# Optimization experiments

Measured on AMD Instinct MI355X. Metric: run time of the kernel, lower is better.

Reference implementation:

```python
import jax, jax.numpy as jnp
import numpy as np

B, T, D1, D2, DM, V, K = 2, 512, 256, 128, 1024, 32000, 4
SCALE = 0.05  # keep tanh/sigmoid out of full saturation with randn params


def setup_inputs() -> dict:
    key = jax.random.key(0)
    ks = jax.random.split(key, 7)
    s = lambda k, shape: SCALE * jax.random.normal(k, shape, dtype=jnp.float32)
    return {
        "gc": jax.random.normal(ks[0], (B, T, D1), dtype=jnp.float32),
        "H": s(ks[1], (K, DM, D1)),
        "U": s(ks[2], (K, D2, D1)),
        "v": s(ks[3], (V, D2)),
        "u": s(ks[4], (K, D1)),
        "b": s(ks[5], (V, K)),
        "emb": s(ks[6], (V, DM)),
    }


def reference(gc, H, U, v, u, b, emb):
    # gc: (B,T,D1)
    hc = jnp.tanh(jnp.einsum('kdi,bti->btkd', H, gc))        # (B,T,K,DM)
    tU = jnp.tanh(jnp.einsum('kji,bti->btkj', U, gc))        # (B,T,K,D2)
    # token- and context-dependent gate logits: (B,T,V,K)
    lc = (jnp.einsum('vj,btkj->btvk', v, tU)
          + jnp.einsum('ki,bti->btk', u, gc)[:, :, None, :]
          + b[None, None])
    gamma = jax.nn.sigmoid(lc[..., :K - 1])                  # (B,T,V,3)
    g0, g1, g2 = gamma[..., 0], gamma[..., 1], gamma[..., 2]
    # sigmoid-tree mixture priors: (B,T,V,K)
    pi = jnp.stack([g0 * g1, g0 * (1.0 - g1),
                    (1.0 - g0) * g2, (1.0 - g0) * (1.0 - g2)], axis=-1)
    # contract hc with embeddings per gate FIRST (avoids btikj blow-up),
    # then weight by pi -- same math as the original pi (x) emb outer product.
    dots = jnp.einsum('btkd,vd->btvk', hc, emb)              # (B,T,V,K)
    logits = jnp.sum(pi * dots, axis=-1)                     # (B,T,V)
    return jax.nn.softmax(logits, axis=-1)
```

## Files before the change

### kernel.cpp

```cpp
#include <hip/hip_runtime.h>
#include <math.h>

namespace {

typedef _Float16 f16;
typedef _Float16 f16x8 __attribute__((ext_vector_type(8)));
typedef float    f32x4 __attribute__((ext_vector_type(4)));

constexpr int kBT = 1024, kD1 = 256, kD2 = 128, kDM = 1024, kV = 32000, kK = 4;
constexpr int AR = kBT * kK;
constexpr int ROWS_H = kK * kDM;
constexpr int ROWS_U = kK * kD2;
constexpr int ROWS_ALL = ROWS_H + ROWS_U + kK;
constexpr int HALF_ROWS = ROWS_ALL / 2;

__global__ __launch_bounds__(256) void prep_gemm(
    const float* __restrict__ gc, const float* __restrict__ Hm,
    const float* __restrict__ Um, const float* __restrict__ um,
    f16* __restrict__ hc, f16* __restrict__ tu, float* __restrict__ ug)
{
    __shared__ float sgc[8][kD1];
    const int btBase = blockIdx.x * 8;
    for (int idx = threadIdx.x; idx < 8 * kD1; idx += 256)
        sgc[idx / kD1][idx % kD1] = gc[(size_t)btBase * kD1 + idx];
    __syncthreads();

    const int rStart = blockIdx.y * HALF_ROWS;
    const int rEnd   = rStart + HALF_ROWS;
    for (int r = rStart + (int)threadIdx.x; r < rEnd; r += 256) {
        const float* wrow;
        if (r < ROWS_H)               wrow = Hm + (size_t)r * kD1;
        else if (r < ROWS_H + ROWS_U) wrow = Um + (size_t)(r - ROWS_H) * kD1;
        else                          wrow = um + (size_t)(r - ROWS_H - ROWS_U) * kD1;

        float acc[8] = {0.f,0.f,0.f,0.f,0.f,0.f,0.f,0.f};
        for (int i = 0; i < kD1; i += 4) {
            const float4 w = *reinterpret_cast<const float4*>(wrow + i);
            #pragma unroll
            for (int b = 0; b < 8; ++b) {
                const float4 g = *reinterpret_cast<const float4*>(&sgc[b][i]);
                acc[b] = fmaf(w.x, g.x, acc[b]);
                acc[b] = fmaf(w.y, g.y, acc[b]);
                acc[b] = fmaf(w.z, g.z, acc[b]);
                acc[b] = fmaf(w.w, g.w, acc[b]);
            }
        }
        #pragma unroll
        for (int b = 0; b < 8; ++b) {
            const int bt = btBase + b;
            if (r < ROWS_H) {
                const int k = r >> 10, d = r & 1023;
                hc[((size_t)(bt * kK + k) << 10) + d] = (f16)tanhf(acc[b]);
            } else if (r < ROWS_H + ROWS_U) {
                const int r2 = r - ROWS_H;
                const int k = r2 >> 7, j = r2 & 127;
                tu[(size_t)(bt * kK + k) * kD2 + j] = (f16)tanhf(acc[b]);
            } else {
                ug[bt * kK + (r - ROWS_H - ROWS_U)] = acc[b];
            }
        }
    }
}

__global__ __launch_bounds__(256) void cvt_kernel(
    const float* __restrict__ src, f16* __restrict__ dst, int n8)
{
    const int i = blockIdx.x * 256 + threadIdx.x;
    if (i >= n8) return;
    const float4 x0 = *reinterpret_cast<const float4*>(src + (size_t)i * 8);
    const float4 x1 = *reinterpret_cast<const float4*>(src + (size_t)i * 8 + 4);
    union { f16 h[8]; uint4 v; } u;
    u.h[0] = (f16)x0.x; u.h[1] = (f16)x0.y; u.h[2] = (f16)x0.z; u.h[3] = (f16)x0.w;
    u.h[4] = (f16)x1.x; u.h[5] = (f16)x1.y; u.h[6] = (f16)x1.z; u.h[7] = (f16)x1.w;
    *reinterpret_cast<uint4*>(dst + (size_t)i * 8) = u.v;
}

__device__ __forceinline__ uint packf16x2(float a, float b) {
    union { f16 h[2]; uint u; } z;
    z.h[0] = (f16)a; z.h[1] = (f16)b;
    return z.u;
}

__global__ __launch_bounds__(256, 2) void fused_mfma(
    const f16* __restrict__ hc,  const f16* __restrict__ tu,
    const f16* __restrict__ v16, const f16* __restrict__ e16,
    const float* __restrict__ ug, const float* __restrict__ bmat,
    float* __restrict__ out)
{
    __shared__ __align__(16) f16 sA[2][128 * 64];
    __shared__ __align__(16) f16 sB[2][128 * 64];

    constexpr int NT_G = kD2 / 64;
    constexpr int NT   = NT_G + kDM / 64;

    const int tid  = threadIdx.x;
    const int lane = tid & 63;
    const int wave = tid >> 6;
    const int fr = lane & 15, fq = lane >> 4;
    const int wrow = wave >> 1, wcol = wave & 1;
    const int aRowBase = blockIdx.x * 128;
    const int vBase    = blockIdx.y * 128;

    const int srow = lane >> 3;
    const int scol = ((lane & 7) ^ srow) * 8;

    auto stage_tile = [&](int t) {
        const bool g = (t < NT_G);
        const f16* A = g ? tu  : hc;
        const f16* B = g ? v16 : e16;
        const int stride = g ? kD2 : kDM;
        const int dB = g ? t * 64 : (t - NT_G) * 64;
        f16* da = &sA[t & 1][0];
        f16* db = &sB[t & 1][0];
        #pragma unroll
        for (int i = 0; i < 4; ++i) {
            const int c = wave * 4 + i;
            const f16* srcA = A + (size_t)(aRowBase + c * 8 + srow) * stride + dB + scol;
            __builtin_amdgcn_global_load_lds(
                (const __attribute__((address_space(1))) void*)srcA,
                (__attribute__((address_space(3))) void*)(da + c * 512), 16, 0, 0);
            const f16* srcB = B + (size_t)(vBase + c * 8 + srow) * stride + dB + scol;
            __builtin_amdgcn_global_load_lds(
                (const __attribute__((address_space(1))) void*)srcB,
                (__attribute__((address_space(3))) void*)(db + c * 512), 16, 0, 0);
        }
    };

    auto mmStep = [&](f32x4 (&acc)[4][4], int q) {
        const f16* __restrict__ pa = &sA[q][0];
        const f16* __restrict__ pb = &sB[q][0];
        #pragma unroll
        for (int kk = 0; kk < 2; ++kk) {
            f16x8 a[4], b[4];
            #pragma unroll
            for (int m = 0; m < 4; ++m) {
                const int r = wrow * 64 + m * 16 + fr;
                const int ps = (kk * 4 + fq) ^ (r & 7);
                a[m] = *reinterpret_cast<const f16x8*>(pa + r * 64 + ps * 8);
            }
            #pragma unroll
            for (int n = 0; n < 4; ++n) {
                const int r = wcol * 64 + n * 16 + fr;
                const int ps = (kk * 4 + fq) ^ (r & 7);
                b[n] = *reinterpret_cast<const f16x8*>(pb + r * 64 + ps * 8);
            }
            #pragma unroll
            for (int m = 0; m < 4; ++m)
                #pragma unroll
                for (int n = 0; n < 4; ++n)
                    acc[m][n] = __builtin_amdgcn_mfma_f32_16x16x32_f16(
                        a[m], b[n], acc[m][n], 0, 0, 0);
        }
    };

    const f32x4 zz = {0.f, 0.f, 0.f, 0.f};

    f32x4 gacc[4][4];
    #pragma unroll
    for (int m = 0; m < 4; ++m)
        #pragma unroll
        for (int n = 0; n < 4; ++n) gacc[m][n] = zz;

    stage_tile(0);
    for (int t = 0; t < NT_G; ++t) {
        stage_tile(t + 1);
        asm volatile("s_waitcnt vmcnt(8)" ::: "memory");
        __builtin_amdgcn_s_barrier();
        mmStep(gacc, t & 1);
        asm volatile("" ::: "memory");
        __builtin_amdgcn_s_barrier();
    }

    uint pi01[4][4], pi23[4][4];
    {
        const int btB = blockIdx.x * 32 + wrow * 16;
        #pragma unroll
        for (int m = 0; m < 4; ++m) {
            const float4 ugv = *reinterpret_cast<const float4*>(ug + (btB + m * 4 + fq) * 4);
            #pragma unroll
            for (int n = 0; n < 4; ++n) {
                const int v = vBase + wcol * 64 + n * 16 + fr;
                const float4 bb = *reinterpret_cast<const float4*>(bmat + (size_t)v * 4);
                const float l0 = gacc[m][n][0] + ugv.x + bb.x;
                const float l1 = gacc[m][n][1] + ugv.y + bb.y;
                const float l2 = gacc[m][n][2] + ugv.z + bb.z;
                const float g0 = 1.f / (1.f + __expf(-l0));
                const float g1 = 1.f / (1.f + __expf(-l1));
                const float g2 = 1.f / (1.f + __expf(-l2));
                pi01[m][n] = packf16x2(g0 * g1, g0 * (1.f - g1));
                pi23[m][n] = packf16x2((1.f - g0) * g2, (1.f - g0) * (1.f - g2));
            }
        }
    }

    f32x4 dacc[4][4];
    #pragma unroll
    for (int m = 0; m < 4; ++m)
        #pragma unroll
        for (int n = 0; n < 4; ++n) dacc[m][n] = zz;

    for (int t = NT_G; t < NT - 1; ++t) {
        stage_tile(t + 1);
        asm volatile("s_waitcnt vmcnt(8)" ::: "memory");
        __builtin_amdgcn_s_barrier();
        mmStep(dacc, t & 1);
        asm volatile("" ::: "memory");
        __builtin_amdgcn_s_barrier();
    }
    asm volatile("s_waitcnt vmcnt(0)" ::: "memory");
    __builtin_amdgcn_s_barrier();
    mmStep(dacc, (NT - 1) & 1);

    const int btB = blockIdx.x * 32 + wrow * 16;
    #pragma unroll
    for (int m = 0; m < 4; ++m) {
        const int bt = btB + m * 4 + fq;
        #pragma unroll
        for (int n = 0; n < 4; ++n) {
            const int v = vBase + wcol * 64 + n * 16 + fr;
            union { uint u; f16 h[2]; } p01, p23;
            p01.u = pi01[m][n]; p23.u = pi23[m][n];
            const float lg = (float)p01.h[0] * dacc[m][n][0]
                           + (float)p01.h[1] * dacc[m][n][1]
                           + (float)p23.h[0] * dacc[m][n][2]
                           + (float)p23.h[1] * dacc[m][n][3];
            out[(size_t)bt * kV + v] = lg;
        }
    }
}

__global__ __launch_bounds__(256) void softmax_kernel(float* __restrict__ out)
{
    __shared__ float red[4];
    float* row = out + (size_t)blockIdx.x * kV;
    const int tid = threadIdx.x;

    float s = 0.f;
    for (int i = tid * 4; i < kV; i += 1024) {
        const float4 x = *reinterpret_cast<const float4*>(row + i);
        s += __expf(x.x) + __expf(x.y) + __expf(x.z) + __expf(x.w);
    }
    #pragma unroll
    for (int o = 1; o < 64; o <<= 1) s += __shfl_xor(s, o);
    if ((tid & 63) == 0) red[tid >> 6] = s;
    __syncthreads();
    s = red[0] + red[1] + red[2] + red[3];
    const float inv = 1.f / s;

    for (int i = tid * 4; i < kV; i += 1024) {
        const float4 x = *reinterpret_cast<const float4*>(row + i);
        float4 y;
        y.x = __expf(x.x) * inv;
        y.y = __expf(x.y) * inv;
        y.z = __expf(x.z) * inv;
        y.w = __expf(x.w) * inv;
        *reinterpret_cast<float4*>(row + i) = y;
    }
}

}

extern "C" void kernel_launch(void* const* d_in, const int* in_sizes, int n_in,
                              void* d_out, int out_size, void* d_ws, size_t ws_size,
                              hipStream_t stream)
{
    (void)in_sizes; (void)n_in; (void)out_size; (void)ws_size;
    const float* gc   = (const float*)d_in[0];
    const float* Hm   = (const float*)d_in[1];
    const float* Um   = (const float*)d_in[2];
    const float* vmat = (const float*)d_in[3];
    const float* um   = (const float*)d_in[4];
    const float* bmat = (const float*)d_in[5];
    const float* emb  = (const float*)d_in[6];
    float* out = (float*)d_out;

    size_t off = 0;
    auto take = [&](size_t bytes) -> char* {
        char* p = (char*)d_ws + off;
        off += (bytes + 255) & ~(size_t)255;
        return p;
    };
    f16*   hc  = (f16*)  take((size_t)AR * kDM * 2);
    f16*   tu  = (f16*)  take((size_t)AR * kD2 * 2);
    f16*   v16 = (f16*)  take((size_t)kV * kD2 * 2);
    f16*   e16 = (f16*)  take((size_t)kV * kDM * 2);
    float* ug  = (float*)take((size_t)AR * 4);

    prep_gemm<<<dim3(kBT / 8, 2), 256, 0, stream>>>(gc, Hm, Um, um, hc, tu, ug);
    cvt_kernel<<<(kV * kD2 / 8 + 255) / 256, 256, 0, stream>>>(vmat, v16, kV * kD2 / 8);
    cvt_kernel<<<(kV * kDM / 8 + 255) / 256, 256, 0, stream>>>(emb, e16, kV * kDM / 8);
    fused_mfma<<<dim3(AR / 128, kV / 128), 256, 0, stream>>>(
        hc, tu, v16, e16, ug, bmat, out);
    softmax_kernel<<<dim3(kBT), 256, 0, stream>>>(out);
}
```

Measured before the change: 560.3 us.

## Fuse softmax exp-sum into GEMM epilogue and precompute LDS fragment addresses

The GEMM epilogue now computes exp of each logit, reduces it across the 16-lane group, and writes per-block partial sums to a workspace buffer. The softmax kernel reads these partials instead of re-reading and exponentiating the whole 32000-wide row, which removes one full pass over the 131 MB output. The mmStep LDS addressing is also hoisted into precomputed base pointers, with s_setprio raised around the MFMA bursts, and the bias loads are hoisted out of the m loop. The cost is extra epilogue exp/shuffle work and a small psum buffer. Since no max is subtracted, it relies on logits being small enough not to overflow exp, as the softmax already did.

```diff
diff --git a/kernel.cpp b/kernel.cpp
--- a/kernel.cpp
+++ b/kernel.cpp
@@ -13,6 +13,7 @@
 constexpr int ROWS_U = kK * kD2;
 constexpr int ROWS_ALL = ROWS_H + ROWS_U + kK;
 constexpr int HALF_ROWS = ROWS_ALL / 2;
+constexpr int NBY = kV / 128;
 
 __global__ __launch_bounds__(256) void prep_gemm(
     const float* __restrict__ gc, const float* __restrict__ Hm,
@@ -85,7 +86,7 @@
     const f16* __restrict__ hc,  const f16* __restrict__ tu,
     const f16* __restrict__ v16, const f16* __restrict__ e16,
     const float* __restrict__ ug, const float* __restrict__ bmat,
-    float* __restrict__ out)
+    float* __restrict__ out, float* __restrict__ psum)
 {
     __shared__ __align__(16) f16 sA[2][128 * 64];
     __shared__ __align__(16) f16 sB[2][128 * 64];
@@ -100,6 +101,7 @@
     const int wrow = wave >> 1, wcol = wave & 1;
     const int aRowBase = blockIdx.x * 128;
     const int vBase    = blockIdx.y * 128;
+    const int btB      = blockIdx.x * 32 + wrow * 16;
 
     const int srow = lane >> 3;
     const int scol = ((lane & 7) ^ srow) * 8;
@@ -126,30 +128,48 @@
         }
     };
 
+    const int ps0 = (fq ^ (fr & 7)) * 8;
+    const int ps1 = ((4 + fq) ^ (fr & 7)) * 8;
+    const f16* rA0 = &sA[0][0] + (wrow * 64 + fr) * 64 + ps0;
+    const f16* rA1 = &sA[0][0] + (wrow * 64 + fr) * 64 + ps1;
+    const f16* rB0 = &sB[0][0] + (wcol * 64 + fr) * 64 + ps0;
+    const f16* rB1 = &sB[0][0] + (wcol * 64 + fr) * 64 + ps1;
+
     auto mmStep = [&](f32x4 (&acc)[4][4], int q) {
-        const f16* __restrict__ pa = &sA[q][0];
-        const f16* __restrict__ pb = &sB[q][0];
-        #pragma unroll
-        for (int kk = 0; kk < 2; ++kk) {
+        const int qo = q * 8192;
+        {
             f16x8 a[4], b[4];
             #pragma unroll
-            for (int m = 0; m < 4; ++m) {
-                const int r = wrow * 64 + m * 16 + fr;
-                const int ps = (kk * 4 + fq) ^ (r & 7);
-                a[m] = *reinterpret_cast<const f16x8*>(pa + r * 64 + ps * 8);
-            }
-            #pragma unroll
-            for (int n = 0; n < 4; ++n) {
-                const int r = wcol * 64 + n * 16 + fr;
-                const int ps = (kk * 4 + fq) ^ (r & 7);
-                b[n] = *reinterpret_cast<const f16x8*>(pb + r * 64 + ps * 8);
-            }
+            for (int m = 0; m < 4; ++m)
+                a[m] = *reinterpret_cast<const f16x8*>(rA0 + qo + m * 1024);
+            #pragma unroll
+            for (int n = 0; n < 4; ++n)
+                b[n] = *reinterpret_cast<const f16x8*>(rB0 + qo + n * 1024);
+            __builtin_amdgcn_s_setprio(1);
             #pragma unroll
             for (int m = 0; m < 4; ++m)
                 #pragma unroll
                 for (int n = 0; n < 4; ++n)
                     acc[m][n] = __builtin_amdgcn_mfma_f32_16x16x32_f16(
                         a[m], b[n], acc[m][n], 0, 0, 0);
+            __builtin_amdgcn_s_setprio(0);
+        }
+        {
+            f16x8 a[4], b[4];
+            #pragma unroll
+            for (int m = 0; m < 4; ++m)
+                a[m] = *reinterpret_cast<const f16x8*>(rA1 + qo + m * 1024);
+            #pragma unroll
+            for (int n = 0; n < 4; ++n)
+                b[n] = *reinterpret_cast<const f16x8*>(rB1 + qo + n * 1024);
+            __builtin_amdgcn_s_setprio(1);
+            #pragma unroll
+            for (int m = 0; m < 4; ++m)
+                #pragma unroll
+                for (int n = 0; n < 4; ++n)
+                    acc[m][n] = __builtin_amdgcn_mfma_f32_16x16x32_f16(
+                        a[m], b[n], acc[m][n], 0, 0, 0);
+            __builtin_amdgcn_s_setprio(0);
         }
     };
 
@@ -173,17 +193,20 @@
 
     uint pi01[4][4], pi23[4][4];
     {
-        const int btB = blockIdx.x * 32 + wrow * 16;
+        float4 bb[4];
+        #pragma unroll
+        for (int n = 0; n < 4; ++n)
+            bb[n] = *reinterpret_cast<const float4*>(
+                bmat + (size_t)(vBase + wcol * 64 + n * 16 + fr) * 4);
         #pragma unroll
         for (int m = 0; m < 4; ++m) {
-            const float4 ugv = *reinterpret_cast<const float4*>(ug + (btB + m * 4 + fq) * 4);
+            const float4 ugv = *reinterpret_cast<const float4*>(
+                ug + (btB + m * 4 + fq) * 4);
             #pragma unroll
             for (int n = 0; n < 4; ++n) {
-                const int v = vBase + wcol * 64 + n * 16 + fr;
-                const float4 bb = *reinterpret_cast<const float4*>(bmat + (size_t)v * 4);
-                const float l0 = gacc[m][n][0] + ugv.x + bb.x;
-                const float l1 = gacc[m][n][1] + ugv.y + bb.y;
-                const float l2 = gacc[m][n][2] + ugv.z + bb.z;
+                const float l0 = gacc[m][n][0] + ugv.x + bb[n].x;
+                const float l1 = gacc[m][n][1] + ugv.y + bb[n].y;
+                const float l2 = gacc[m][n][2] + ugv.z + bb[n].z;
                 const float g0 = 1.f / (1.f + __expf(-l0));
                 const float g1 = 1.f / (1.f + __expf(-l1));
                 const float g2 = 1.f / (1.f + __expf(-l2));
@@ -211,10 +234,10 @@
     __builtin_amdgcn_s_barrier();
     mmStep(dacc, (NT - 1) & 1);
 
-    const int btB = blockIdx.x * 32 + wrow * 16;
     #pragma unroll
     for (int m = 0; m < 4; ++m) {
         const int bt = btB + m * 4 + fq;
+        float es = 0.f;
         #pragma unroll
         for (int n = 0; n < 4; ++n) {
             const int v = vBase + wcol * 64 + n * 16 + fr;
@@ -225,21 +248,27 @@
                            + (float)p23.h[0] * dacc[m][n][2]
                            + (float)p23.h[1] * dacc[m][n][3];
             out[(size_t)bt * kV + v] = lg;
-        }
-    }
-}
-
-__global__ __launch_bounds__(256) void softmax_kernel(float* __restrict__ out)
+            es += __expf(lg);
+        }
+        es += __shfl_xor(es, 1);
+        es += __shfl_xor(es, 2);
+        es += __shfl_xor(es, 4);
+        es += __shfl_xor(es, 8);
+        if (fr == 0)
+            psum[(size_t)bt * 512 + blockIdx.y * 2 + wcol] = es;
+    }
+}
+
+__global__ __launch_bounds__(256) void softmax_kernel(
+    float* __restrict__ out, const float* __restrict__ psum)
 {
     __shared__ float red[4];
-    float* row = out + (size_t)blockIdx.x * kV;
+    const int bt = blockIdx.x;
+    float* row = out + (size_t)bt * kV;
     const int tid = threadIdx.x;
 
     float s = 0.f;
-    for (int i = tid * 4; i < kV; i += 1024) {
-        const float4 x = *reinterpret_cast<const float4*>(row + i);
-        s += __expf(x.x) + __expf(x.y) + __expf(x.z) + __expf(x.w);
-    }
+    for (int i = tid; i < 2 * NBY; i += 256) s += psum[(size_t)bt * 512 + i];
     #pragma unroll
     for (int o = 1; o < 64; o <<= 1) s += __shfl_xor(s, o);
     if ((tid & 63) == 0) red[tid >> 6] = s;
@@ -280,16 +309,17 @@
         off += (bytes + 255) & ~(size_t)255;
         return p;
     };
-    f16*   hc  = (f16*)  take((size_t)AR * kDM * 2);
-    f16*   tu  = (f16*)  take((size_t)AR * kD2 * 2);
-    f16*   v16 = (f16*)  take((size_t)kV * kD2 * 2);
-    f16*   e16 = (f16*)  take((size_t)kV * kDM * 2);
-    float* ug  = (float*)take((size_t)AR * 4);
+    f16*   hc   = (f16*)  take((size_t)AR * kDM * 2);
+    f16*   tu   = (f16*)  take((size_t)AR * kD2 * 2);
+    f16*   v16  = (f16*)  take((size_t)kV * kD2 * 2);
+    f16*   e16  = (f16*)  take((size_t)kV * kDM * 2);
+    float* ug   = (float*)take((size_t)AR * 4);
+    float* psum = (float*)take((size_t)kBT * 512 * 4);
 
     prep_gemm<<<dim3(kBT / 8, 2), 256, 0, stream>>>(gc, Hm, Um, um, hc, tu, ug);
     cvt_kernel<<<(kV * kD2 / 8 + 255) / 256, 256, 0, stream>>>(vmat, v16, kV * kD2 / 8);
     cvt_kernel<<<(kV * kDM / 8 + 255) / 256, 256, 0, stream>>>(emb, e16, kV * kDM / 8);
-    fused_mfma<<<dim3(AR / 128, kV / 128), 256, 0, stream>>>(
-        hc, tu, v16, e16, ug, bmat, out);
-    softmax_kernel<<<dim3(kBT), 256, 0, stream>>>(out);
-}
+    fused_mfma<<<dim3(AR / 128, NBY), 256, 0, stream>>>(
+        hc, tu, v16, e16, ug, bmat, out, psum);
+    softmax_kernel<<<dim3(kBT), 256, 0, stream>>>(out, psum);
+}
```

Result: no change. 561.4 us (+0.2%).
